# Optimization experiments

Measured on AMD Instinct MI355X. Metric: run time of the kernel, lower is better.

## Reference

```python
import jax, jax.numpy as jnp
import numpy as np

DIM = 1024
H = 8
HK = DIM // H  # head key dim = 128 (expand_k=1.0)
HV = DIM // H  # head value dim = 128 (expand_v=1.0)
GLR = 16       # gate low-rank dim (fla default)
GATE_LOGIT_NORMALIZER = 16.0
EPS = 1e-5
B, T = 2, 512


def setup_inputs() -> dict:
    key = jax.random.key(0)
    ks = jax.random.split(key, 9)
    s = lambda k, shp: jax.random.normal(k, shp, jnp.float32) * (shp[0] ** -0.5)
    return {
        "x": jax.random.normal(ks[0], (B, T, DIM), jnp.float32),
        "Wq": s(ks[1], (DIM, DIM)),
        "Wk": s(ks[2], (DIM, DIM)),
        "Wv": s(ks[3], (DIM, DIM)),
        "Wg": s(ks[4], (DIM, DIM)),
        "Wgk1": s(ks[5], (DIM, GLR)),
        "Wgk2": s(ks[6], (GLR, DIM)),
        "bgk2": jnp.zeros((DIM,), jnp.float32),
        "g_norm_w": jnp.ones((HV,), jnp.float32),
        "Wo": s(ks[7], (DIM, DIM)),
    }


def _gla_forward(x, Wq, Wk, Wv, Wg, Wgk1, Wgk2, bgk2, g_norm_w, Wo):
    b, t, _ = x.shape
    # projections
    q = (x @ Wq).reshape(b, t, H, HK) * (HK ** -0.5)
    k = (x @ Wk).reshape(b, t, H, HK)
    v = (x @ Wv).reshape(b, t, H, HV)
    # low-rank forget gate: logsigmoid / normalizer, per key channel
    gk = (jax.nn.log_sigmoid((x @ Wgk1) @ Wgk2 + bgk2) / GATE_LOGIT_NORMALIZER)
    gk = gk.reshape(b, t, H, HK)

    # recurrent decay-gated linear attention:
    #   S_t = diag(exp(gk_t)) @ S_{t-1} + k_t^T v_t ; o_t = q_t @ S_t
    def step(h, inp):
        qt, kt, vt, gt = inp  # each [B, H, HK] / [B, H, HV]
        h = h * jnp.exp(gt)[..., None] + kt[..., None] * vt[..., None, :]
        ot = jnp.einsum("bhk,bhkv->bhv", qt, h)
        return h, ot

    h0 = jnp.zeros((b, H, HK, HV), x.dtype)
    xs = (
        q.transpose(1, 0, 2, 3),
        k.transpose(1, 0, 2, 3),
        v.transpose(1, 0, 2, 3),
        gk.transpose(1, 0, 2, 3),
    )
    _, o = jax.lax.scan(step, h0, xs)  # o: [T, B, H, HV]
    o = o.transpose(1, 0, 2, 3)        # [B, T, H, HV]

    # gated RMSNorm with swish gate over per-head value dim, then output proj
    g = (x @ Wg).reshape(b, t, H, HV)
    rms = jax.lax.rsqrt(jnp.mean(o * o, axis=-1, keepdims=True) + EPS)
    o = (o * rms) * g_norm_w * (g * jax.nn.sigmoid(g))
    return o.reshape(b, t, DIM) @ Wo


def reference(x, Wq, Wk, Wv, Wg, Wgk1, Wgk2, bgk2, g_norm_w, Wo):
    return _gla_forward(x, Wq, Wk, Wv, Wg, Wgk1, Wgk2, bgk2, g_norm_w, Wo)
```

## Files before the change

### kernel.cpp

```cpp
#include <hip/hip_runtime.h>
#include <hip/hip_bf16.h>
#include <math.h>

#define BT     1024
#define NH     8
#define SEGLEN 32
#define NSEG   16
#define NBH    16
#define QKS    136
#define VTS    40
#define AMS    40

typedef __attribute__((ext_vector_type(8))) short short8;
typedef __attribute__((ext_vector_type(4))) short sh4;
typedef __attribute__((ext_vector_type(4))) float f32x4;

__device__ __forceinline__ float bitf(short u) {
    union { float f; unsigned i; } x; x.i = ((unsigned)(unsigned short)u) << 16; return x.f;
}
__device__ __forceinline__ short f2bf(float f) {
    union { float f; unsigned u; } x; x.f = f;
    unsigned r = x.u + 0x7FFF + ((x.u >> 16) & 1);
    return (short)(r >> 16);
}
__device__ __forceinline__ void gload_lds16(const short* g, short* l) {
    __builtin_amdgcn_global_load_lds(
        (const __attribute__((address_space(1))) unsigned int*)g,
        (__attribute__((address_space(3))) unsigned int*)l, 16, 0, 0);
}

__global__ __launch_bounds__(256) void cast_all(
    const float* __restrict__ Wq, const float* __restrict__ Wk,
    const float* __restrict__ Wv, const float* __restrict__ Wg,
    const float* __restrict__ Wo, const float* __restrict__ X,
    short* __restrict__ WT, short* __restrict__ Xb)
{
    const int z = blockIdx.z;
    const int tid = threadIdx.x;
    if (z == 5) {
        const int id = blockIdx.y * 32 + blockIdx.x;
        const int i = id * 1024 + tid * 4;
        float4 a = *(const float4*)(X + i);
        sh4 v;
        v[0] = f2bf(a.x); v[1] = f2bf(a.y); v[2] = f2bf(a.z); v[3] = f2bf(a.w);
        *(sh4*)(Xb + i) = v;
        return;
    }
    const float* W = (z == 0) ? Wq : (z == 1) ? Wk : (z == 2) ? Wv : (z == 3) ? Wg : Wo;
    short* T = WT + (size_t)z * (1u << 20);
    __shared__ float tile[32][33];
    const int k0 = blockIdx.y * 32, n0 = blockIdx.x * 32;
    const int row = tid >> 3, c4 = (tid & 7) << 2;
    float4 f = *(const float4*)(W + (size_t)(k0 + row) * 1024 + n0 + c4);
    tile[row][c4 + 0] = f.x; tile[row][c4 + 1] = f.y;
    tile[row][c4 + 2] = f.z; tile[row][c4 + 3] = f.w;
    __syncthreads();
    short* o = T + (size_t)(n0 + row) * 1024 + k0 + c4;
    o[0] = f2bf(tile[c4 + 0][row]); o[1] = f2bf(tile[c4 + 1][row]);
    o[2] = f2bf(tile[c4 + 2][row]); o[3] = f2bf(tile[c4 + 3][row]);
}

__global__ __launch_bounds__(256) void proj_gk(
    const short* __restrict__ Xb, const short* __restrict__ WT,
    short* __restrict__ QKVG,
    const float* __restrict__ Wgk1, const float* __restrict__ Wgk2,
    const float* __restrict__ bgk2, short* __restrict__ GK)
{
    const int z = blockIdx.z;
    const int tid = threadIdx.x;
    const int wave = tid >> 6, lane = tid & 63;

    if (z == 4) {
        const int row = (blockIdx.y * 16 + blockIdx.x) * 4 + wave;
        float p[16];
        #pragma unroll
        for (int j = 0; j < 16; j++) p[j] = 0.f;
        for (int d8 = 0; d8 < 16; d8++) {
            const int d = d8 * 64 + lane;
            float xv = bitf(Xb[(size_t)row * 1024 + d]);
            #pragma unroll
            for (int j = 0; j < 16; j++)
                p[j] = fmaf(xv, Wgk1[d * 16 + j], p[j]);
        }
        #pragma unroll
        for (int j = 0; j < 16; j++)
            #pragma unroll
            for (int off = 32; off; off >>= 1)
                p[j] += __shfl_xor(p[j], off);
        for (int c8 = 0; c8 < 16; c8++) {
            const int c = c8 * 64 + lane;
            float acc = bgk2[c];
            #pragma unroll
            for (int j = 0; j < 16; j++)
                acc = fmaf(p[j], Wgk2[j * 1024 + c], acc);
            float ls = fminf(acc, 0.f) - log1pf(expf(-fabsf(acc)));
            GK[(size_t)row * 1024 + c] = f2bf(ls * (1.f / 16.f));
        }
        return;
    }

    const float scale = (z == 0) ? 0.08838834764831845f : 1.0f;
    short* C = QKVG + (size_t)z * (1u << 20);
    const short* B = WT + (size_t)z * (1u << 20);

    __shared__ __align__(16) short As[8 * 64 * 8];
    __shared__ __align__(16) short Bs[8 * 64 * 8];
    const int wm = (wave >> 1) * 32, wn = (wave & 1) * 32;
    const int m15 = lane & 15, q = lane >> 4;
    const int m0 = blockIdx.y * 64, n0 = blockIdx.x * 64;

    f32x4 acc[2][2];
    #pragma unroll
    for (int i = 0; i < 2; i++)
        #pragma unroll
        for (int j = 0; j < 2; j++)
            acc[i][j] = (f32x4){0.f, 0.f, 0.f, 0.f};

    for (int kb0 = 0; kb0 < 1024; kb0 += 64) {
        __syncthreads();
        #pragma unroll
        for (int c = 0; c < 2; c++) {
            const int k8 = wave * 2 + c;
            gload_lds16(Xb + (size_t)(m0 + lane) * 1024 + kb0 + k8 * 8, &As[(k8 * 64) * 8]);
            gload_lds16(B  + (size_t)(n0 + lane) * 1024 + kb0 + k8 * 8, &Bs[(k8 * 64) * 8]);
        }
        __syncthreads();
        #pragma unroll
        for (int s = 0; s < 2; s++) {
            const int k8 = s * 4 + q;
            short8 af[2], bf[2];
            #pragma unroll
            for (int i = 0; i < 2; i++)
                af[i] = *(const short8*)&As[(k8 * 64 + wm + i * 16 + m15) * 8];
            #pragma unroll
            for (int j = 0; j < 2; j++)
                bf[j] = *(const short8*)&Bs[(k8 * 64 + wn + j * 16 + m15) * 8];
            #pragma unroll
            for (int i = 0; i < 2; i++)
                #pragma unroll
                for (int j = 0; j < 2; j++)
                    acc[i][j] = __builtin_amdgcn_mfma_f32_16x16x32_bf16(af[i], bf[j], acc[i][j], 0, 0, 0);
        }
    }
    #pragma unroll
    for (int i = 0; i < 2; i++)
        #pragma unroll
        for (int j = 0; j < 2; j++)
            #pragma unroll
            for (int rr = 0; rr < 4; rr++)
                C[(size_t)(m0 + wm + i * 16 + q * 4 + rr) * 1024 + n0 + wn + j * 16 + m15] =
                    f2bf(acc[i][j][rr] * scale);
}

__global__ __launch_bounds__(256) void wo_gemm(
    const short* __restrict__ A, const short* __restrict__ B, float* __restrict__ C)
{
    __shared__ __align__(16) short As[8 * 64 * 8];
    __shared__ __align__(16) short Bs[8 * 64 * 8];
    const int tid = threadIdx.x;
    const int wave = tid >> 6, lane = tid & 63;
    const int wm = (wave >> 1) * 32, wn = (wave & 1) * 32;
    const int m15 = lane & 15, q = lane >> 4;
    const int m0 = blockIdx.y * 64, n0 = blockIdx.x * 64;

    f32x4 acc[2][2];
    #pragma unroll
    for (int i = 0; i < 2; i++)
        #pragma unroll
        for (int j = 0; j < 2; j++)
            acc[i][j] = (f32x4){0.f, 0.f, 0.f, 0.f};

    for (int kb0 = 0; kb0 < 1024; kb0 += 64) {
        __syncthreads();
        #pragma unroll
        for (int c = 0; c < 2; c++) {
            const int k8 = wave * 2 + c;
            gload_lds16(A + (size_t)(m0 + lane) * 1024 + kb0 + k8 * 8, &As[(k8 * 64) * 8]);
            gload_lds16(B + (size_t)(n0 + lane) * 1024 + kb0 + k8 * 8, &Bs[(k8 * 64) * 8]);
        }
        __syncthreads();
        #pragma unroll
        for (int s = 0; s < 2; s++) {
            const int k8 = s * 4 + q;
            short8 af[2], bf[2];
            #pragma unroll
            for (int i = 0; i < 2; i++)
                af[i] = *(const short8*)&As[(k8 * 64 + wm + i * 16 + m15) * 8];
            #pragma unroll
            for (int j = 0; j < 2; j++)
                bf[j] = *(const short8*)&Bs[(k8 * 64 + wn + j * 16 + m15) * 8];
            #pragma unroll
            for (int i = 0; i < 2; i++)
                #pragma unroll
                for (int j = 0; j < 2; j++)
                    acc[i][j] = __builtin_amdgcn_mfma_f32_16x16x32_bf16(af[i], bf[j], acc[i][j], 0, 0, 0);
        }
    }
    #pragma unroll
    for (int i = 0; i < 2; i++)
        #pragma unroll
        for (int j = 0; j < 2; j++)
            #pragma unroll
            for (int rr = 0; rr < 4; rr++)
                C[(size_t)(m0 + wm + i * 16 + q * 4 + rr) * 1024 + n0 + wn + j * 16 + m15] =
                    acc[i][j][rr];
}

__global__ __launch_bounds__(256) void scan_chunk(
    const short* __restrict__ Q, const short* __restrict__ K,
    const short* __restrict__ V, short* GKQT,
    short* __restrict__ O, short* __restrict__ SS, float* __restrict__ DSEG)
{
    const int seg = blockIdx.x;
    const int bh  = blockIdx.y;
    const int b = bh >> 3, h = bh & 7;
    const int tid = threadIdx.x;
    const int wave = tid >> 6, lane = tid & 63;
    const size_t rowbase = (size_t)(b * 512 + seg * SEGLEN) * 1024 + h * 128;

    __shared__ __align__(16) short Qt[32 * QKS];
    __shared__ __align__(16) short Kt[32 * QKS];
    __shared__ __align__(16) short Vs[32 * 128];
    __shared__ __align__(16) short VT[128 * VTS];
    __shared__ __align__(16) short KhT[128 * VTS];
    __shared__ __align__(16) short Am[32 * AMS];
    __shared__ float htot[2][128];

    #pragma unroll
    for (int c = 0; c < 2; c++) {
        const int fb = (wave * 2 + c) * 64;
        const int f = fb + lane;
        const int t = f >> 4, c8 = f & 15;
        gload_lds16(V + rowbase + (size_t)t * 1024 + c8 * 8, &Vs[fb * 8]);
    }

    const int ch = tid & 127, th2 = tid >> 7;
    float g[16], kv[16], qv[16];
    #pragma unroll
    for (int tt = 0; tt < 16; tt++) {
        const size_t a = rowbase + (size_t)(th2 * 16 + tt) * 1024 + ch;
        g[tt] = bitf(GKQT[a]); kv[tt] = bitf(K[a]); qv[tt] = bitf(Q[a]);
    }
    float run = 0.f;
    #pragma unroll
    for (int tt = 0; tt < 16; tt++) { run += g[tt]; g[tt] = run; }
    htot[th2][ch] = run;
    __syncthreads();
    const float base_ = th2 ? htot[0][ch] : 0.f;
    const float eGend = expf(htot[0][ch] + htot[1][ch]);
    if (th2 == 0) DSEG[(bh * NSEG + seg) * 128 + ch] = eGend;
    #pragma unroll
    for (int tt = 0; tt < 16; tt++) {
        const int t = th2 * 16 + tt;
        const size_t a = rowbase + (size_t)t * 1024 + ch;
        const float Gc = base_ + g[tt];
        const float eg = expf(Gc);
        short qts = f2bf(qv[tt] * eg);
        Qt[t * QKS + ch] = qts;
        GKQT[a] = qts;
        float ktv = kv[tt] * expf(-Gc);
        Kt[t * QKS + ch] = f2bf(ktv);
        KhT[ch * VTS + t] = f2bf(ktv * eGend);
    }
    __syncthreads();
    {
        const int vch = tid >> 1, t0 = (tid & 1) * 16;
        #pragma unroll
        for (int j = 0; j < 4; j++) {
            sh4 p;
            p[0] = Vs[(t0 + 4 * j + 0) * 128 + vch];
            p[1] = Vs[(t0 + 4 * j + 1) * 128 + vch];
            p[2] = Vs[(t0 + 4 * j + 2) * 128 + vch];
            p[3] = Vs[(t0 + 4 * j + 3) * 128 + vch];
            *(sh4*)&VT[vch * VTS + t0 + 4 * j] = p;
        }
    }
    __syncthreads();

    const int m15 = lane & 15, q = lane >> 4;

    {
        const int mi = wave >> 1, ni = wave & 1;
        f32x4 a1 = (f32x4){0.f, 0.f, 0.f, 0.f};
        #pragma unroll
        for (int kc = 0; kc < 4; kc++) {
            short8 af = *(const short8*)&Qt[(mi * 16 + m15) * QKS + kc * 32 + q * 8];
            short8 bf = *(const short8*)&Kt[(ni * 16 + m15) * QKS + kc * 32 + q * 8];
            a1 = __builtin_amdgcn_mfma_f32_16x16x32_bf16(af, bf, a1, 0, 0, 0);
        }
        #pragma unroll
        for (int rr = 0; rr < 4; rr++) {
            const int t = mi * 16 + q * 4 + rr, s = ni * 16 + m15;
            Am[t * AMS + s] = (t >= s) ? f2bf(a1[rr]) : (short)0;
        }
    }
    __syncthreads();

    {
        const int mi = wave >> 1, nb = (wave & 1) * 4;
        short8 af = *(const short8*)&Am[(mi * 16 + m15) * AMS + q * 8];
        #pragma unroll
        for (int jj = 0; jj < 4; jj++) {
            short8 bf = *(const short8*)&VT[((nb + jj) * 16 + m15) * VTS + q * 8];
            f32x4 a2 = (f32x4){0.f, 0.f, 0.f, 0.f};
            a2 = __builtin_amdgcn_mfma_f32_16x16x32_bf16(af, bf, a2, 0, 0, 0);
            #pragma unroll
            for (int rr = 0; rr < 4; rr++)
                O[rowbase + (size_t)(mi * 16 + q * 4 + rr) * 1024 + (nb + jj) * 16 + m15] =
                    f2bf(a2[rr]);
        }
    }

    {
        const size_t sbase = (size_t)(bh * NSEG + seg) * 16384;
        #pragma unroll
        for (int m2 = 0; m2 < 2; m2++) {
            const int mrow = wave * 2 + m2;
            short8 af = *(const short8*)&VT[(mrow * 16 + m15) * VTS + q * 8];
            #pragma unroll
            for (int ni = 0; ni < 8; ni++) {
                short8 bf = *(const short8*)&KhT[(ni * 16 + m15) * VTS + q * 8];
                f32x4 a3 = (f32x4){0.f, 0.f, 0.f, 0.f};
                a3 = __builtin_amdgcn_mfma_f32_16x16x32_bf16(af, bf, a3, 0, 0, 0);
                #pragma unroll
                for (int rr = 0; rr < 4; rr++)
                    SS[sbase + (size_t)(mrow * 16 + q * 4 + rr) * 128 + ni * 16 + m15] =
                        f2bf(a3[rr]);
            }
        }
    }
}

__global__ __launch_bounds__(256) void stitch(
    short* __restrict__ SS, const float* __restrict__ DSEG)
{
    const int slice = blockIdx.x;
    const int bh = blockIdx.y, tid = threadIdx.x;
    __shared__ float dloc[NSEG][128];
    for (int i = tid; i < NSEG * 128; i += 256)
        dloc[i >> 7][i & 127] = DSEG[(bh * NSEG + (i >> 7)) * 128 + (i & 127)];
    __syncthreads();
    const int kch0 = (tid * 2) & 127;
    float run[2][2] = {{0.f, 0.f}, {0.f, 0.f}};
    for (int seg = 0; seg < NSEG; seg++) {
        const size_t base = (size_t)(bh * NSEG + seg) * 16384 + slice * 1024;
        const float d0 = dloc[seg][kch0], d1 = dloc[seg][kch0 + 1];
        #pragma unroll
        for (int j = 0; j < 2; j++) {
            unsigned* p = (unsigned*)&SS[base + j * 512 + tid * 2];
            unsigned u = *p;
            float t0 = bitf((short)(u & 0xFFFF));
            float t1 = bitf((short)(u >> 16));
            unsigned w0 = (unsigned short)f2bf(run[j][0]);
            unsigned w1 = (unsigned short)f2bf(run[j][1]);
            *p = w0 | (w1 << 16);
            run[j][0] = fmaf(run[j][0], d0, t0);
            run[j][1] = fmaf(run[j][1], d1, t1);
        }
    }
}

__global__ __launch_bounds__(256) void corr_gnorm(
    const short* __restrict__ QT, const short* __restrict__ SS,
    const short* __restrict__ O, const short* __restrict__ G,
    const float* __restrict__ gnw, short* __restrict__ Obf)
{
    const int seg = blockIdx.x;
    const int bh = blockIdx.y;
    const int b = bh >> 3, h = bh & 7;
    const int tid = threadIdx.x;
    const int wave = tid >> 6, lane = tid & 63;
    const int m15 = lane & 15, q = lane >> 4;
    const size_t rowbase = (size_t)(b * 512 + seg * SEGLEN) * 1024 + h * 128;
    const size_t sbase = (size_t)(bh * NSEG + seg) * 16384;

    __shared__ __align__(16) short Qs[16 * 32 * 8];
    __shared__ __align__(16) short Ss[16 * 128 * 8];
    __shared__ __align__(16) short Gs[16 * 32 * 8];
    __shared__ __align__(16) short Os[16 * 32 * 8];
    __shared__ float red[4][16];

    #pragma unroll
    for (int c = 0; c < 2; c++) {
        const int fb = (wave * 2 + c) * 64;
        const int f = fb + lane;
        const int k8 = f >> 5, t = f & 31;
        gload_lds16(QT + rowbase + (size_t)t * 1024 + k8 * 8, &Qs[fb * 8]);
    }
    #pragma unroll
    for (int c = 0; c < 2; c++) {
        const int fb = (wave * 2 + c) * 64;
        const int f = fb + lane;
        const int v8 = f >> 5, t = f & 31;
        gload_lds16(G + rowbase + (size_t)t * 1024 + v8 * 8, &Gs[fb * 8]);
        gload_lds16(O + rowbase + (size_t)t * 1024 + v8 * 8, &Os[fb * 8]);
    }
    #pragma unroll
    for (int c = 0; c < 8; c++) {
        const int fb = wave * 512 + c * 64;
        const int f = fb + lane;
        const int k8 = f >> 7, vch = f & 127;
        gload_lds16(SS + sbase + (size_t)vch * 128 + k8 * 8, &Ss[fb * 8]);
    }
    __syncthreads();

    const int mt = wave >> 1, nh2 = wave & 1;
    f32x4 acc[4];
    #pragma unroll
    for (int nt = 0; nt < 4; nt++) acc[nt] = (f32x4){0.f, 0.f, 0.f, 0.f};
    #pragma unroll
    for (int kb = 0; kb < 4; kb++) {
        short8 af = *(const short8*)&Qs[((kb * 4 + q) * 32 + mt * 16 + m15) * 8];
        #pragma unroll
        for (int nt = 0; nt < 4; nt++) {
            short8 bf = *(const short8*)&Ss[((kb * 4 + q) * 128 + nh2 * 64 + nt * 16 + m15) * 8];
            acc[nt] = __builtin_amdgcn_mfma_f32_16x16x32_bf16(af, bf, acc[nt], 0, 0, 0);
        }
    }

    float o[4][4];
    float ssq[4] = {0.f, 0.f, 0.f, 0.f};
    #pragma unroll
    for (int nt = 0; nt < 4; nt++) {
        const int vch = nh2 * 64 + nt * 16 + m15;
        #pragma unroll
        for (int rr = 0; rr < 4; rr++) {
            const int t = mt * 16 + q * 4 + rr;
            float ov = bitf(Os[((vch >> 3) * 32 + t) * 8 + (vch & 7)]) + acc[nt][rr];
            o[nt][rr] = ov;
            ssq[rr] = fmaf(ov, ov, ssq[rr]);
        }
    }
    #pragma unroll
    for (int rr = 0; rr < 4; rr++) {
        ssq[rr] += __shfl_xor(ssq[rr], 1);
        ssq[rr] += __shfl_xor(ssq[rr], 2);
        ssq[rr] += __shfl_xor(ssq[rr], 4);
        ssq[rr] += __shfl_xor(ssq[rr], 8);
    }
    if (m15 == 0) {
        #pragma unroll
        for (int rr = 0; rr < 4; rr++) red[wave][q * 4 + rr] = ssq[rr];
    }
    __syncthreads();
    float rsq[4];
    #pragma unroll
    for (int rr = 0; rr < 4; rr++) {
        float ms = (red[wave][q * 4 + rr] + red[wave ^ 1][q * 4 + rr]) * (1.f / 128.f);
        rsq[rr] = rsqrtf(ms + 1e-5f);
    }
    #pragma unroll
    for (int nt = 0; nt < 4; nt++) {
        const int vch = nh2 * 64 + nt * 16 + m15;
        const float gw = gnw[vch];
        #pragma unroll
        for (int rr = 0; rr < 4; rr++) {
            const int t = mt * 16 + q * 4 + rr;
            float g = bitf(Gs[((vch >> 3) * 32 + t) * 8 + (vch & 7)]);
            float sg = g / (1.f + expf(-g));
            Obf[rowbase + (size_t)t * 1024 + vch] = f2bf(o[nt][rr] * rsq[rr] * gw * sg);
        }
    }
}

extern "C" void kernel_launch(void* const* d_in, const int* in_sizes, int n_in,
                              void* d_out, int out_size, void* d_ws, size_t ws_size,
                              hipStream_t stream)
{
    const float* X    = (const float*)d_in[0];
    const float* Wq   = (const float*)d_in[1];
    const float* Wk   = (const float*)d_in[2];
    const float* Wv   = (const float*)d_in[3];
    const float* Wg   = (const float*)d_in[4];
    const float* Wgk1 = (const float*)d_in[5];
    const float* Wgk2 = (const float*)d_in[6];
    const float* bgk2 = (const float*)d_in[7];
    const float* gnw  = (const float*)d_in[8];
    const float* Wo   = (const float*)d_in[9];
    float* OUT = (float*)d_out;

    short* QKVG = (short*)d_ws;
    short* GK   = QKVG + (4u << 20);
    short* Ob   = GK + (1u << 20);
    short* SS   = Ob + (1u << 20);
    float* DS   = (float*)(SS + (4u << 20));
    short* WT   = (short*)(DS + 32768);
    short* Xb   = WT + (5u << 20);
    short* Obf  = QKVG;

    cast_all<<<dim3(32, 32, 6), 256, 0, stream>>>(Wq, Wk, Wv, Wg, Wo, X, WT, Xb);
    proj_gk<<<dim3(16, 16, 5), 256, 0, stream>>>(Xb, WT, QKVG, Wgk1, Wgk2, bgk2, GK);
    scan_chunk<<<dim3(NSEG, NBH), 256, 0, stream>>>(
        QKVG, QKVG + (1u << 20), QKVG + (2u << 20), GK, Ob, SS, DS);
    stitch<<<dim3(16, NBH), 256, 0, stream>>>(SS, DS);
    corr_gnorm<<<dim3(NSEG, NBH), 256, 0, stream>>>(
        GK, SS, Ob, QKVG + (3u << 20), gnw, Obf);
    wo_gemm<<<dim3(16, 16), 256, 0, stream>>>(Obf, WT + (4u << 20), OUT);
}
```

Measured before the change: 174.1 us.

## Split gate projection into own kernel and widen QKVG GEMM tile to 64x128

Pulls the low-rank gate computation out of the projection kernel into a dedicated kernel with one block per row. It uses a transposed bf16 copy of Wgk1 for coalesced loads and reduces across the whole block. The QKVG GEMM tile grows from 64x64 to 64x128, halving the block count and increasing B-operand reuse per block. The cost is one extra kernel launch, an extra cast slice, fewer GEMM blocks (512 vs 1024), and more registers per thread.

```diff
diff --git a/kernel.cpp b/kernel.cpp
--- a/kernel.cpp
+++ b/kernel.cpp
@@ -33,7 +33,8 @@
     const float* __restrict__ Wq, const float* __restrict__ Wk,
     const float* __restrict__ Wv, const float* __restrict__ Wg,
     const float* __restrict__ Wo, const float* __restrict__ X,
-    short* __restrict__ WT, short* __restrict__ Xb)
+    const float* __restrict__ Wgk1,
+    short* __restrict__ WT, short* __restrict__ Xb, short* __restrict__ Wgk1T)
 {
     const int z = blockIdx.z;
     const int tid = threadIdx.x;
@@ -46,6 +47,17 @@
         *(sh4*)(Xb + i) = v;
         return;
     }
+    if (z == 6) {
+        const int id = blockIdx.y * 32 + blockIdx.x;
+        if (id >= 16) return;
+        const int d = id * 64 + (tid & 63), jj = tid >> 6;
+        float4 w = *(const float4*)(Wgk1 + d * 16 + jj * 4);
+        Wgk1T[(jj * 4 + 0) * 1024 + d] = f2bf(w.x);
+        Wgk1T[(jj * 4 + 1) * 1024 + d] = f2bf(w.y);
+        Wgk1T[(jj * 4 + 2) * 1024 + d] = f2bf(w.z);
+        Wgk1T[(jj * 4 + 3) * 1024 + d] = f2bf(w.w);
+        return;
+    }
     const float* W = (z == 0) ? Wq : (z == 1) ? Wk : (z == 2) ? Wv : (z == 3) ? Wg : Wo;
     short* T = WT + (size_t)z * (1u << 20);
     __shared__ float tile[32][33];
@@ -60,60 +72,28 @@
     o[2] = f2bf(tile[c4 + 2][row]); o[3] = f2bf(tile[c4 + 3][row]);
 }
 
-__global__ __launch_bounds__(256) void proj_gk(
+__global__ __launch_bounds__(256) void proj_gemm(
     const short* __restrict__ Xb, const short* __restrict__ WT,
-    short* __restrict__ QKVG,
-    const float* __restrict__ Wgk1, const float* __restrict__ Wgk2,
-    const float* __restrict__ bgk2, short* __restrict__ GK)
+    short* __restrict__ QKVG)
 {
     const int z = blockIdx.z;
-    const int tid = threadIdx.x;
-    const int wave = tid >> 6, lane = tid & 63;
-
-    if (z == 4) {
-        const int row = (blockIdx.y * 16 + blockIdx.x) * 4 + wave;
-        float p[16];
-        #pragma unroll
-        for (int j = 0; j < 16; j++) p[j] = 0.f;
-        for (int d8 = 0; d8 < 16; d8++) {
-            const int d = d8 * 64 + lane;
-            float xv = bitf(Xb[(size_t)row * 1024 + d]);
-            #pragma unroll
-            for (int j = 0; j < 16; j++)
-                p[j] = fmaf(xv, Wgk1[d * 16 + j], p[j]);
-        }
-        #pragma unroll
-        for (int j = 0; j < 16; j++)
-            #pragma unroll
-            for (int off = 32; off; off >>= 1)
-                p[j] += __shfl_xor(p[j], off);
-        for (int c8 = 0; c8 < 16; c8++) {
-            const int c = c8 * 64 + lane;
-            float acc = bgk2[c];
-            #pragma unroll
-            for (int j = 0; j < 16; j++)
-                acc = fmaf(p[j], Wgk2[j * 1024 + c], acc);
-            float ls = fminf(acc, 0.f) - log1pf(expf(-fabsf(acc)));
-            GK[(size_t)row * 1024 + c] = f2bf(ls * (1.f / 16.f));
-        }
-        return;
-    }
-
     const float scale = (z == 0) ? 0.08838834764831845f : 1.0f;
     short* C = QKVG + (size_t)z * (1u << 20);
     const short* B = WT + (size_t)z * (1u << 20);
 
     __shared__ __align__(16) short As[8 * 64 * 8];
-    __shared__ __align__(16) short Bs[8 * 64 * 8];
-    const int wm = (wave >> 1) * 32, wn = (wave & 1) * 32;
+    __shared__ __align__(16) short Bs[8 * 128 * 8];
+    const int tid = threadIdx.x;
+    const int wave = tid >> 6, lane = tid & 63;
+    const int wm = (wave >> 1) * 32, wn = (wave & 1) * 64;
     const int m15 = lane & 15, q = lane >> 4;
-    const int m0 = blockIdx.y * 64, n0 = blockIdx.x * 64;
-
-    f32x4 acc[2][2];
+    const int m0 = blockIdx.y * 64, n0 = blockIdx.x * 128;
+
+    f32x4 acc[2][4];
     #pragma unroll
     for (int i = 0; i < 2; i++)
         #pragma unroll
-        for (int j = 0; j < 2; j++)
+        for (int j = 0; j < 4; j++)
             acc[i][j] = (f32x4){0.f, 0.f, 0.f, 0.f};
 
     for (int kb0 = 0; kb0 < 1024; kb0 += 64) {
@@ -121,31 +101,35 @@
         #pragma unroll
         for (int c = 0; c < 2; c++) {
             const int k8 = wave * 2 + c;
-            gload_lds16(Xb + (size_t)(m0 + lane) * 1024 + kb0 + k8 * 8, &As[(k8 * 64) * 8]);
-            gload_lds16(B  + (size_t)(n0 + lane) * 1024 + kb0 + k8 * 8, &Bs[(k8 * 64) * 8]);
+            gload_lds16(Xb + (size_t)(m0 + lane) * 1024 + kb0 + k8 * 8,
+                        &As[(k8 * 64) * 8]);
+            #pragma unroll
+            for (int rh = 0; rh < 2; rh++)
+                gload_lds16(B + (size_t)(n0 + rh * 64 + lane) * 1024 + kb0 + k8 * 8,
+                            &Bs[(k8 * 128 + rh * 64) * 8]);
         }
         __syncthreads();
         #pragma unroll
         for (int s = 0; s < 2; s++) {
             const int k8 = s * 4 + q;
-            short8 af[2], bf[2];
+            short8 af[2], bf[4];
             #pragma unroll
             for (int i = 0; i < 2; i++)
                 af[i] = *(const short8*)&As[(k8 * 64 + wm + i * 16 + m15) * 8];
             #pragma unroll
-            for (int j = 0; j < 2; j++)
-                bf[j] = *(const short8*)&Bs[(k8 * 64 + wn + j * 16 + m15) * 8];
+            for (int j = 0; j < 4; j++)
+                bf[j] = *(const short8*)&Bs[(k8 * 128 + wn + j * 16 + m15) * 8];
             #pragma unroll
             for (int i = 0; i < 2; i++)
                 #pragma unroll
-                for (int j = 0; j < 2; j++)
+                for (int j = 0; j < 4; j++)
                     acc[i][j] = __builtin_amdgcn_mfma_f32_16x16x32_bf16(af[i], bf[j], acc[i][j], 0, 0, 0);
         }
     }
     #pragma unroll
     for (int i = 0; i < 2; i++)
         #pragma unroll
-        for (int j = 0; j < 2; j++)
+        for (int j = 0; j < 4; j++)
             #pragma unroll
             for (int rr = 0; rr < 4; rr++)
                 C[(size_t)(m0 + wm + i * 16 + q * 4 + rr) * 1024 + n0 + wn + j * 16 + m15] =
@@ -204,6 +188,45 @@
             for (int rr = 0; rr < 4; rr++)
                 C[(size_t)(m0 + wm + i * 16 + q * 4 + rr) * 1024 + n0 + wn + j * 16 + m15] =
                     acc[i][j][rr];
+}
+
+__global__ __launch_bounds__(256) void gk_proj(
+    const short* __restrict__ Xb, const short* __restrict__ Wgk1T,
+    const float* __restrict__ Wgk2, const float* __restrict__ bgk2,
+    short* __restrict__ GK)
+{
+    const int row = blockIdx.x, tid = threadIdx.x;
+    const int d4 = tid * 4;
+    sh4 xv = *(const sh4*)(Xb + (size_t)row * 1024 + d4);
+    float x0 = bitf(xv[0]), x1 = bitf(xv[1]), x2 = bitf(xv[2]), x3 = bitf(xv[3]);
+    float p[16];
+    #pragma unroll
+    for (int j = 0; j < 16; j++) {
+        sh4 w = *(const sh4*)(Wgk1T + j * 1024 + d4);
+        p[j] = x0 * bitf(w[0]) + x1 * bitf(w[1]) + x2 * bitf(w[2]) + x3 * bitf(w[3]);
+    }
+    #pragma unroll
+    for (int j = 0; j < 16; j++)
+        #pragma unroll
+        for (int off = 32; off; off >>= 1) p[j] += __shfl_xor(p[j], off);
+    __shared__ float zp[4][16];
+    __shared__ float z[16];
+    const int lane = tid & 63, w = tid >> 6;
+    if (lane == 0) {
+        #pragma unroll
+        for (int j = 0; j < 16; j++) zp[w][j] = p[j];
+    }
+    __syncthreads();
+    if (tid < 16) z[tid] = zp[0][tid] + zp[1][tid] + zp[2][tid] + zp[3][tid];
+    __syncthreads();
+    for (int c = tid; c < 1024; c += 256) {
+        float acc = bgk2[c];
+        #pragma unroll
+        for (int j = 0; j < 16; j++)
+            acc = fmaf(z[j], Wgk2[j * 1024 + c], acc);
+        float ls = fminf(acc, 0.f) - log1pf(expf(-fabsf(acc)));
+        GK[(size_t)row * 1024 + c] = f2bf(ls * (1.f / 16.f));
+    }
 }
 
 __global__ __launch_bounds__(256) void scan_chunk(
@@ -479,17 +502,19 @@
     const float* Wo   = (const float*)d_in[9];
     float* OUT = (float*)d_out;
 
-    short* QKVG = (short*)d_ws;
-    short* GK   = QKVG + (4u << 20);
-    short* Ob   = GK + (1u << 20);
-    short* SS   = Ob + (1u << 20);
-    float* DS   = (float*)(SS + (4u << 20));
-    short* WT   = (short*)(DS + 32768);
-    short* Xb   = WT + (5u << 20);
-    short* Obf  = QKVG;
-
-    cast_all<<<dim3(32, 32, 6), 256, 0, stream>>>(Wq, Wk, Wv, Wg, Wo, X, WT, Xb);
-    proj_gk<<<dim3(16, 16, 5), 256, 0, stream>>>(Xb, WT, QKVG, Wgk1, Wgk2, bgk2, GK);
+    short* QKVG  = (short*)d_ws;
+    short* GK    = QKVG + (4u << 20);
+    short* Ob    = GK + (1u << 20);
+    short* SS    = Ob + (1u << 20);
+    float* DS    = (float*)(SS + (4u << 20));
+    short* WT    = (short*)(DS + 32768);
+    short* Xb    = WT + (5u << 20);
+    short* Wgk1T = Xb + (1u << 20);
+    short* Obf   = QKVG;
+
+    cast_all<<<dim3(32, 32, 7), 256, 0, stream>>>(Wq, Wk, Wv, Wg, Wo, X, Wgk1, WT, Xb, Wgk1T);
+    proj_gemm<<<dim3(8, 16, 4), 256, 0, stream>>>(Xb, WT, QKVG);
+    gk_proj<<<dim3(BT), 256, 0, stream>>>(Xb, Wgk1T, Wgk2, bgk2, GK);
     scan_chunk<<<dim3(NSEG, NBH), 256, 0, stream>>>(
         QKVG, QKVG + (1u << 20), QKVG + (2u << 20), GK, Ob, SS, DS);
     stitch<<<dim3(16, NBH), 256, 0, stream>>>(SS, DS);
```

After: 158.4 us (median of 3 runs). -9.0%, faster.
